# Kernel optimization log

Hardware: AMD Instinct MI355X
Metric: run time of the kernel (lower is better)

The kernel has to match this reference:

```python
import jax, jax.numpy as jnp
import numpy as np
import math

B, I, O, SEG = 128, 2048, 2048, 10

def setup_inputs() -> dict:
    key = jax.random.key(0)
    k1, k2, k3, k4 = jax.random.split(key, 4)
    scale = 1.0 / math.sqrt(I)
    return {
        "x": jax.random.normal(k1, (B, I), dtype=jnp.float32),
        "context": jax.random.normal(k2, (O,), dtype=jnp.float32),
        "prev_activation": jax.random.normal(k3, (B, O), dtype=jnp.float32),
        "weight": jax.random.normal(k4, (O, I), dtype=jnp.float32) * scale,
        "bias": jnp.zeros((O,), dtype=jnp.float32),
        "astrocyte_activation": jnp.ones((O,), dtype=jnp.float32),
        "dendrite_segments": jax.random.normal(jax.random.fold_in(key, 7), (O, I, SEG), dtype=jnp.float32) * scale,
    }

def reference(x, context, prev_activation, weight, bias, astrocyte_activation, dendrite_segments):
    # Astrocyte gating of the linear weight: sigmoid(astro * context) -> [o]
    astro_mod = jax.nn.sigmoid(astrocyte_activation * context)
    # Dendritic branch: relu(einsum('bi,oij->boj')) summed over segments -> [b, o]
    dendritic_out = jnp.maximum(jnp.einsum('bi,oij->boj', x, dendrite_segments), 0.0).sum(axis=2)
    # Gated linear: F.linear(x, weight * astro_mod[:, None], bias) -> [b, o]
    out = x @ (weight * astro_mod[:, None]).T + bias
    # Note: torch's STDP/Hebbian weight mutations (synaptic_tag, protein_synthesis,
    # homeostatic scaling) occur AFTER 'out' is computed and do not affect the
    # returned tensor; they are pure parameter side effects, so omitted here.
    return out + dendritic_out
```

## Files before the change

kernel.cpp:

```cpp
#include <hip/hip_runtime.h>
#include <hip/hip_bf16.h>

#define B_ 128
#define I_ 2048
#define O_ 2048
#define SEG 10
#define BK 32
#define NST (I_ / BK)
#define XTILE 8192
#define DCH 1280
#define DLS 1408

typedef __attribute__((ext_vector_type(8))) short bf16x8;
typedef __attribute__((ext_vector_type(4))) float f32x4;

static __device__ __forceinline__ unsigned short f2bf(float f) {
    unsigned u = __float_as_uint(f);
    u += 0x7FFFu + ((u >> 16) & 1u);
    return (unsigned short)(u >> 16);
}

static __device__ __forceinline__ unsigned cvt2(float lo, float hi) {
    __hip_bfloat162 h = __float22bfloat162_rn(make_float2(lo, hi));
    return *reinterpret_cast<unsigned*>(&h);
}

#define GLDS16(SRC, DST) \
    __builtin_amdgcn_global_load_lds( \
        (const __attribute__((address_space(1))) unsigned*)(SRC), \
        (__attribute__((address_space(3))) unsigned*)(DST), 16, 0, 0)
#define GLDS4(SRC, DST) \
    __builtin_amdgcn_global_load_lds( \
        (const __attribute__((address_space(1))) unsigned*)(SRC), \
        (__attribute__((address_space(3))) unsigned*)(DST), 4, 0, 0)

#define WAITVM(N) asm volatile("s_waitcnt vmcnt(" #N ")" ::: "memory")
#define BARRIER() do { __builtin_amdgcn_sched_barrier(0); \
                       __builtin_amdgcn_s_barrier(); \
                       __builtin_amdgcn_sched_barrier(0); } while (0)

__global__ void xconv(const float* __restrict__ x, char* __restrict__ xb) {
    int idx = blockIdx.x * 256 + threadIdx.x;
    int row = idx >> 8;
    int c   = idx & 255;
    int k0  = c * 8;
    int tt  = k0 >> 5;
    int kl  = k0 & 31;

    const float* xp = x + (size_t)row * I_ + k0;
    float4 a = *reinterpret_cast<const float4*>(xp);
    float4 b = *reinterpret_cast<const float4*>(xp + 4);

    bf16x8 h;
    h[0] = (short)f2bf(a.x); h[1] = (short)f2bf(a.y);
    h[2] = (short)f2bf(a.z); h[3] = (short)f2bf(a.w);
    h[4] = (short)f2bf(b.x); h[5] = (short)f2bf(b.y);
    h[6] = (short)f2bf(b.z); h[7] = (short)f2bf(b.w);

    int sw = ((row >> 1) & 3) << 4;
    size_t off = (size_t)tt * XTILE + row * 64 + ((kl * 2) ^ sw);
    *reinterpret_cast<bf16x8*>(xb + off) = h;
}

__global__ __launch_bounds__(256, 2) void neuro_fused(
    const char*  __restrict__ xb,
    const float* __restrict__ ctx,
    const float* __restrict__ w,
    const float* __restrict__ bias,
    const float* __restrict__ astro,
    const float* __restrict__ D,
    float* __restrict__ out)
{
    __shared__ __align__(16) char xs[4][XTILE];
    __shared__ __align__(16) char dls[4][4][DLS];

    const int tid  = threadIdx.x;
    const int wv   = tid >> 6;
    const int lane = tid & 63;
    const bool isP = (wv < 2);
    const int o0   = blockIdx.x * 4;
    const int col  = lane & 15;
    const int g    = lane >> 4;

    const int p = wv;
    auto stage_x = [&](int t) {
        const char* src = xb + (size_t)t * XTILE + p * 4096 + lane * 16;
        char* dst = &xs[t & 3][p * 4096];
#pragma unroll
        for (int c = 0; c < 4; ++c)
            GLDS16(src + c * 1024, dst + c * 1024);
    };
    auto stage_d = [&](int t) {
#pragma unroll
        for (int q = 0; q < 2; ++q) {
            const int ol = 2 * p + q;
            const char* srcD = (const char*)D + (size_t)(o0 + ol) * (I_ * SEG * 4)
                             + (size_t)t * DCH;
            char* dst = &dls[ol][t & 3][0];
            GLDS16(srcD + lane * 16, dst);
            GLDS4(srcD + 1024 + lane * 4, dst + 1024);
            const char* srcW = (const char*)w + (size_t)(o0 + ol) * (I_ * 4) + t * (BK * 4);
            if (lane < 32) GLDS4(srcW + lane * 4, dst + DCH);
        }
    };

    const int c_ = wv - 2;
    f32x4 acc[2][8];
#pragma unroll
    for (int oo = 0; oo < 2; ++oo)
#pragma unroll
        for (int m = 0; m < 8; ++m) acc[oo][m] = (f32x4){0.f, 0.f, 0.f, 0.f};

    float am[2], bo[2];
    if (!isP) {
#pragma unroll
        for (int oo = 0; oo < 2; ++oo) {
            const int o = o0 + 2 * c_ + oo;
            float a = astro[o] * ctx[o];
            am[oo] = 1.0f / (1.0f + __expf(-a));
            bo[oo] = bias[o];
        }
    }

    const int fbase = (col < 10) ? col * 4 : DCH;
    const int fstr  = (col < 10) ? 40 : 4;
    const int sw    = ((col >> 1) & 3) << 4;

    auto compute = [&](int u) {
        const char* xbase = &xs[u & 3][0];
        bf16x8 af[8];
#pragma unroll
        for (int m = 0; m < 8; ++m)
            af[m] = *reinterpret_cast<const bf16x8*>(
                xbase + (m * 16 + col) * 64 + ((16 * g) ^ sw));
#pragma unroll
        for (int oo = 0; oo < 2; ++oo) {
            const char* fp = &dls[2 * c_ + oo][u & 3][0] + fbase + (8 * g) * fstr;
            float bv[8];
#pragma unroll
            for (int e = 0; e < 8; ++e)
                bv[e] = *reinterpret_cast<const float*>(fp + e * fstr);
            union { bf16x8 v; unsigned uu[4]; } bf;
#pragma unroll
            for (int e2 = 0; e2 < 4; ++e2)
                bf.uu[e2] = cvt2(bv[2 * e2], bv[2 * e2 + 1]);
#pragma unroll
            for (int m = 0; m < 8; ++m)
                acc[oo][m] = __builtin_amdgcn_mfma_f32_16x16x32_bf16(af[m], bf.v, acc[oo][m], 0, 0, 0);
        }
    };

    if (isP) {
        stage_x(0); stage_d(0);
        stage_x(1); stage_d(1);
        stage_x(2); stage_d(2);
        WAITVM(20);
    }

#pragma unroll 1
    for (int u = 0; u < NST; ++u) {
        BARRIER();
        if (isP) {
            if (u + 3 < NST) { stage_x(u + 3); stage_d(u + 3); }
            if (u <= NST - 4)      { WAITVM(20); }
            else if (u == NST - 3) { WAITVM(10); }
            else                   { WAITVM(0);  }
        } else {
            compute(u);
        }
    }

    if (!isP) {
#pragma unroll
        for (int oo = 0; oo < 2; ++oo) {
            const int o = o0 + 2 * c_ + oo;
#pragma unroll
            for (int m = 0; m < 8; ++m) {
#pragma unroll
                for (int r = 0; r < 4; ++r) {
                    float v = acc[oo][m][r];
                    float dend = (col < 10) ? fmaxf(v, 0.0f) : 0.0f;
#pragma unroll
                    for (int sh = 1; sh < 16; sh <<= 1)
                        dend += __shfl_xor(dend, sh, 64);
                    float lin = __shfl(v, (lane & 48) | 10, 64);
                    if (col == 0) {
                        int b = m * 16 + g * 4 + r;
                        out[(size_t)b * O_ + o] = dend + am[oo] * lin + bo[oo];
                    }
                }
            }
        }
    }
}

extern "C" void kernel_launch(void* const* d_in, const int* in_sizes, int n_in,
                              void* d_out, int out_size, void* d_ws, size_t ws_size,
                              hipStream_t stream) {
    const float* x     = (const float*)d_in[0];
    const float* ctx   = (const float*)d_in[1];
    const float* w     = (const float*)d_in[3];
    const float* bias  = (const float*)d_in[4];
    const float* astro = (const float*)d_in[5];
    const float* D     = (const float*)d_in[6];
    float* out = (float*)d_out;
    char* xb = (char*)d_ws;

    xconv<<<dim3(128), dim3(256), 0, stream>>>(x, xb);
    neuro_fused<<<dim3(512), dim3(256), 0, stream>>>(xb, ctx, w, bias, astro, D, out);
}
```

Before: 48.94 us.

## Replace per-stage block barriers with LDS flag producer/consumer handshakes

The per-stage workgroup barrier is replaced by counters in LDS. The two loader waves publish how many stages are ready, and the two MFMA waves publish how many stages they have consumed. Each side spins with s_sleep on the other's counters, so producers and consumers are no longer locked to each other every iteration and can drift within the 4-deep ring. The cost is polling overhead on volatile LDS reads. Correctness also now relies on the vmcnt wait making the async LDS writes visible to the other waves before a flag is set, which a barrier used to guarantee.

```diff
diff --git a/kernel.cpp b/kernel.cpp
--- a/kernel.cpp
+++ b/kernel.cpp
@@ -35,9 +35,7 @@
         (__attribute__((address_space(3))) unsigned*)(DST), 4, 0, 0)
 
 #define WAITVM(N) asm volatile("s_waitcnt vmcnt(" #N ")" ::: "memory")
-#define BARRIER() do { __builtin_amdgcn_sched_barrier(0); \
-                       __builtin_amdgcn_s_barrier(); \
-                       __builtin_amdgcn_sched_barrier(0); } while (0)
+#define SB() __builtin_amdgcn_sched_barrier(0)
 
 __global__ void xconv(const float* __restrict__ x, char* __restrict__ xb) {
     int idx = blockIdx.x * 256 + threadIdx.x;
@@ -73,6 +71,7 @@
 {
     __shared__ __align__(16) char xs[4][XTILE];
     __shared__ __align__(16) char dls[4][4][DLS];
+    __shared__ int sflg[16];
 
     const int tid  = threadIdx.x;
     const int wv   = tid >> 6;
@@ -82,112 +81,133 @@
     const int col  = lane & 15;
     const int g    = lane >> 4;
 
-    const int p = wv;
-    auto stage_x = [&](int t) {
-        const char* src = xb + (size_t)t * XTILE + p * 4096 + lane * 16;
-        char* dst = &xs[t & 3][p * 4096];
-#pragma unroll
-        for (int c = 0; c < 4; ++c)
-            GLDS16(src + c * 1024, dst + c * 1024);
-    };
-    auto stage_d = [&](int t) {
-#pragma unroll
-        for (int q = 0; q < 2; ++q) {
-            const int ol = 2 * p + q;
-            const char* srcD = (const char*)D + (size_t)(o0 + ol) * (I_ * SEG * 4)
-                             + (size_t)t * DCH;
-            char* dst = &dls[ol][t & 3][0];
-            GLDS16(srcD + lane * 16, dst);
-            GLDS4(srcD + 1024 + lane * 4, dst + 1024);
-            const char* srcW = (const char*)w + (size_t)(o0 + ol) * (I_ * 4) + t * (BK * 4);
-            if (lane < 32) GLDS4(srcW + lane * 4, dst + DCH);
-        }
-    };
-
-    const int c_ = wv - 2;
-    f32x4 acc[2][8];
-#pragma unroll
-    for (int oo = 0; oo < 2; ++oo)
-#pragma unroll
-        for (int m = 0; m < 8; ++m) acc[oo][m] = (f32x4){0.f, 0.f, 0.f, 0.f};
-
-    float am[2], bo[2];
-    if (!isP) {
-#pragma unroll
-        for (int oo = 0; oo < 2; ++oo) {
-            const int o = o0 + 2 * c_ + oo;
-            float a = astro[o] * ctx[o];
-            am[oo] = 1.0f / (1.0f + __expf(-a));
-            bo[oo] = bias[o];
-        }
-    }
-
-    const int fbase = (col < 10) ? col * 4 : DCH;
-    const int fstr  = (col < 10) ? 40 : 4;
-    const int sw    = ((col >> 1) & 3) << 4;
-
-    auto compute = [&](int u) {
-        const char* xbase = &xs[u & 3][0];
-        bf16x8 af[8];
-#pragma unroll
-        for (int m = 0; m < 8; ++m)
-            af[m] = *reinterpret_cast<const bf16x8*>(
-                xbase + (m * 16 + col) * 64 + ((16 * g) ^ sw));
-#pragma unroll
-        for (int oo = 0; oo < 2; ++oo) {
-            const char* fp = &dls[2 * c_ + oo][u & 3][0] + fbase + (8 * g) * fstr;
-            float bv[8];
-#pragma unroll
-            for (int e = 0; e < 8; ++e)
-                bv[e] = *reinterpret_cast<const float*>(fp + e * fstr);
-            union { bf16x8 v; unsigned uu[4]; } bf;
-#pragma unroll
-            for (int e2 = 0; e2 < 4; ++e2)
-                bf.uu[e2] = cvt2(bv[2 * e2], bv[2 * e2 + 1]);
-#pragma unroll
-            for (int m = 0; m < 8; ++m)
-                acc[oo][m] = __builtin_amdgcn_mfma_f32_16x16x32_bf16(af[m], bf.v, acc[oo][m], 0, 0, 0);
-        }
-    };
+    if (tid < 16) sflg[tid] = 0;
+    __syncthreads();
 
     if (isP) {
+        const int p = wv;
+        auto stage_x = [&](int t) {
+            const char* src = xb + (size_t)t * XTILE + p * 4096 + lane * 16;
+            char* dst = &xs[t & 3][p * 4096];
+#pragma unroll
+            for (int c = 0; c < 4; ++c)
+                GLDS16(src + c * 1024, dst + c * 1024);
+        };
+        auto stage_d = [&](int t) {
+#pragma unroll
+            for (int q = 0; q < 2; ++q) {
+                const int ol = 2 * p + q;
+                const char* srcD = (const char*)D + (size_t)(o0 + ol) * (I_ * SEG * 4)
+                                 + (size_t)t * DCH;
+                char* dst = &dls[ol][t & 3][0];
+                GLDS16(srcD + lane * 16, dst);
+                GLDS4(srcD + 1024 + lane * 4, dst + 1024);
+                const char* srcW = (const char*)w + (size_t)(o0 + ol) * (I_ * 4) + t * (BK * 4);
+                if (lane < 32) GLDS4(srcW + lane * 4, dst + DCH);
+            }
+        };
+
         stage_x(0); stage_d(0);
         stage_x(1); stage_d(1);
         stage_x(2); stage_d(2);
-        WAITVM(20);
-    }
+
+        volatile int* vc0 = &sflg[8];
+        volatile int* vc1 = &sflg[12];
+        volatile int* myf = &sflg[p * 4];
 
 #pragma unroll 1
-    for (int u = 0; u < NST; ++u) {
-        BARRIER();
-        if (isP) {
+        for (int u = 0; u < NST; ++u) {
+            while (*vc0 < u || *vc1 < u) {
+                asm volatile("" ::: "memory");
+                __builtin_amdgcn_s_sleep(1);
+            }
+            SB();
             if (u + 3 < NST) { stage_x(u + 3); stage_d(u + 3); }
             if (u <= NST - 4)      { WAITVM(20); }
             else if (u == NST - 3) { WAITVM(10); }
             else                   { WAITVM(0);  }
-        } else {
-            compute(u);
-        }
-    }
-
-    if (!isP) {
+            SB();
+            if (lane == 0) *myf = u + 2;
+        }
+        return;
+    }
+
+    const int c_ = wv - 2;
+    f32x4 acc[2][8];
+#pragma unroll
+    for (int oo = 0; oo < 2; ++oo)
+#pragma unroll
+        for (int m = 0; m < 8; ++m) acc[oo][m] = (f32x4){0.f, 0.f, 0.f, 0.f};
+
+    float am[2], bo[2];
+#pragma unroll
+    for (int oo = 0; oo < 2; ++oo) {
+        const int o = o0 + 2 * c_ + oo;
+        float a = astro[o] * ctx[o];
+        am[oo] = 1.0f / (1.0f + __expf(-a));
+        bo[oo] = bias[o];
+    }
+
+    const int fbase = (col < 10) ? col * 4 : DCH;
+    const int fstr  = (col < 10) ? 40 : 4;
+    const int sw    = ((col >> 1) & 3) << 4;
+
+    auto compute = [&](int u) {
+        const char* xbase = &xs[u & 3][0];
+        bf16x8 af[8];
+#pragma unroll
+        for (int m = 0; m < 8; ++m)
+            af[m] = *reinterpret_cast<const bf16x8*>(
+                xbase + (m * 16 + col) * 64 + ((16 * g) ^ sw));
 #pragma unroll
         for (int oo = 0; oo < 2; ++oo) {
-            const int o = o0 + 2 * c_ + oo;
-#pragma unroll
-            for (int m = 0; m < 8; ++m) {
-#pragma unroll
-                for (int r = 0; r < 4; ++r) {
-                    float v = acc[oo][m][r];
-                    float dend = (col < 10) ? fmaxf(v, 0.0f) : 0.0f;
-#pragma unroll
-                    for (int sh = 1; sh < 16; sh <<= 1)
-                        dend += __shfl_xor(dend, sh, 64);
-                    float lin = __shfl(v, (lane & 48) | 10, 64);
-                    if (col == 0) {
-                        int b = m * 16 + g * 4 + r;
-                        out[(size_t)b * O_ + o] = dend + am[oo] * lin + bo[oo];
-                    }
+            const char* fp = &dls[2 * c_ + oo][u & 3][0] + fbase + (8 * g) * fstr;
+            float bv[8];
+#pragma unroll
+            for (int e = 0; e < 8; ++e)
+                bv[e] = *reinterpret_cast<const float*>(fp + e * fstr);
+            union { bf16x8 v; unsigned uu[4]; } bf;
+#pragma unroll
+            for (int e2 = 0; e2 < 4; ++e2)
+                bf.uu[e2] = cvt2(bv[2 * e2], bv[2 * e2 + 1]);
+#pragma unroll
+            for (int m = 0; m < 8; ++m)
+                acc[oo][m] = __builtin_amdgcn_mfma_f32_16x16x32_bf16(af[m], bf.v, acc[oo][m], 0, 0, 0);
+        }
+    };
+
+    volatile int* vf0 = &sflg[0];
+    volatile int* vf1 = &sflg[4];
+    volatile int* myc = &sflg[8 + c_ * 4];
+
+#pragma unroll 1
+    for (int u = 0; u < NST; ++u) {
+        while (*vf0 < u + 1 || *vf1 < u + 1) {
+            asm volatile("" ::: "memory");
+            __builtin_amdgcn_s_sleep(1);
+        }
+        SB();
+        compute(u);
+        SB();
+        if (lane == 0) *myc = u + 1;
+    }
+
+#pragma unroll
+    for (int oo = 0; oo < 2; ++oo) {
+        const int o = o0 + 2 * c_ + oo;
+#pragma unroll
+        for (int m = 0; m < 8; ++m) {
+#pragma unroll
+            for (int r = 0; r < 4; ++r) {
+                float v = acc[oo][m][r];
+                float dend = (col < 10) ? fmaxf(v, 0.0f) : 0.0f;
+#pragma unroll
+                for (int sh = 1; sh < 16; sh <<= 1)
+                    dend += __shfl_xor(dend, sh, 64);
+                float lin = __shfl(v, (lane & 48) | 10, 64);
+                if (col == 0) {
+                    int b = m * 16 + g * 4 + r;
+                    out[(size_t)b * O_ + o] = dend + am[oo] * lin + bo[oo];
                 }
             }
         }
```

Result: slower. 67.85 us (+38.6%).

## Double K-tile to 64 and widen blocks to 8 outputs with 8 waves

Applied to the files above, without the earlier changes.

Raises the K step per pipeline stage from 32 to 64 and makes each block handle 8 output neurons with 4 producer and 4 consumer waves (512 threads, 256 blocks). This halves the number of barrier-synchronised stages and shares each staged x tile across twice as many outputs. The x layout swizzle and the wait counts are adjusted to match. LDS use grows to about 155 KB and occupancy drops to one block per CU, so less latency is hidden by parallel blocks.

```diff
diff --git a/kernel.cpp b/kernel.cpp
--- a/kernel.cpp
+++ b/kernel.cpp
@@ -5,11 +5,12 @@
 #define I_ 2048
 #define O_ 2048
 #define SEG 10
-#define BK 32
+#define BK 64
 #define NST (I_ / BK)
-#define XTILE 8192
-#define DCH 1280
-#define DLS 1408
+#define XT 16384
+#define DCH 2560
+#define DSL 2816
+#define DEPTH 4
 
 typedef __attribute__((ext_vector_type(8))) short bf16x8;
 typedef __attribute__((ext_vector_type(4))) float f32x4;
@@ -44,8 +45,8 @@
     int row = idx >> 8;
     int c   = idx & 255;
     int k0  = c * 8;
-    int tt  = k0 >> 5;
-    int kl  = k0 & 31;
+    int tt  = k0 >> 6;
+    int kl  = k0 & 63;
 
     const float* xp = x + (size_t)row * I_ + k0;
     float4 a = *reinterpret_cast<const float4*>(xp);
@@ -57,12 +58,11 @@
     h[4] = (short)f2bf(b.x); h[5] = (short)f2bf(b.y);
     h[6] = (short)f2bf(b.z); h[7] = (short)f2bf(b.w);
 
-    int sw = ((row >> 1) & 3) << 4;
-    size_t off = (size_t)tt * XTILE + row * 64 + ((kl * 2) ^ sw);
+    size_t off = (size_t)tt * XT + row * 128 + ((kl * 2) ^ ((row & 7) << 4));
     *reinterpret_cast<bf16x8*>(xb + off) = h;
 }
 
-__global__ __launch_bounds__(256, 2) void neuro_fused(
+__global__ __launch_bounds__(512, 1) void neuro_fused(
     const char*  __restrict__ xb,
     const float* __restrict__ ctx,
     const float* __restrict__ w,
@@ -71,20 +71,20 @@
     const float* __restrict__ D,
     float* __restrict__ out)
 {
-    __shared__ __align__(16) char xs[4][XTILE];
-    __shared__ __align__(16) char dls[4][4][DLS];
+    __shared__ __align__(16) char xs[DEPTH][XT];
+    __shared__ __align__(16) char dls[8][DEPTH][DSL];
 
     const int tid  = threadIdx.x;
     const int wv   = tid >> 6;
     const int lane = tid & 63;
-    const bool isP = (wv < 2);
-    const int o0   = blockIdx.x * 4;
+    const bool isP = (wv < 4);
+    const int o0   = blockIdx.x * 8;
     const int col  = lane & 15;
     const int g    = lane >> 4;
 
     const int p = wv;
     auto stage_x = [&](int t) {
-        const char* src = xb + (size_t)t * XTILE + p * 4096 + lane * 16;
+        const char* src = xb + (size_t)t * XT + p * 4096 + lane * 16;
         char* dst = &xs[t & 3][p * 4096];
 #pragma unroll
         for (int c = 0; c < 4; ++c)
@@ -98,13 +98,15 @@
                              + (size_t)t * DCH;
             char* dst = &dls[ol][t & 3][0];
             GLDS16(srcD + lane * 16, dst);
-            GLDS4(srcD + 1024 + lane * 4, dst + 1024);
+            GLDS16(srcD + 1024 + lane * 16, dst + 1024);
+            GLDS4(srcD + 2048 + lane * 4, dst + 2048);
+            GLDS4(srcD + 2304 + lane * 4, dst + 2304);
             const char* srcW = (const char*)w + (size_t)(o0 + ol) * (I_ * 4) + t * (BK * 4);
-            if (lane < 32) GLDS4(srcW + lane * 4, dst + DCH);
+            GLDS4(srcW + lane * 4, dst + DCH);
         }
     };
 
-    const int c_ = wv - 2;
+    const int c_ = wv - 4;
     f32x4 acc[2][8];
 #pragma unroll
     for (int oo = 0; oo < 2; ++oo)
@@ -124,29 +126,38 @@
 
     const int fbase = (col < 10) ? col * 4 : DCH;
     const int fstr  = (col < 10) ? 40 : 4;
-    const int sw    = ((col >> 1) & 3) << 4;
-
-    auto compute = [&](int u) {
-        const char* xbase = &xs[u & 3][0];
-        bf16x8 af[8];
-#pragma unroll
-        for (int m = 0; m < 8; ++m)
-            af[m] = *reinterpret_cast<const bf16x8*>(
-                xbase + (m * 16 + col) * 64 + ((16 * g) ^ sw));
+    const int sw    = (col & 7) << 4;
+
+    auto compute = [&](int t) {
+        const char* xbase = &xs[t & 3][0];
+        bf16x8 af[2][8];
+#pragma unroll
+        for (int kk = 0; kk < 2; ++kk) {
+            const int kswz = (kk * 64 + 16 * g) ^ sw;
+#pragma unroll
+            for (int m = 0; m < 8; ++m)
+                af[kk][m] = *reinterpret_cast<const bf16x8*>(
+                    xbase + (m * 16 + col) * 128 + kswz);
+        }
 #pragma unroll
         for (int oo = 0; oo < 2; ++oo) {
-            const char* fp = &dls[2 * c_ + oo][u & 3][0] + fbase + (8 * g) * fstr;
-            float bv[8];
-#pragma unroll
-            for (int e = 0; e < 8; ++e)
-                bv[e] = *reinterpret_cast<const float*>(fp + e * fstr);
-            union { bf16x8 v; unsigned uu[4]; } bf;
-#pragma unroll
-            for (int e2 = 0; e2 < 4; ++e2)
-                bf.uu[e2] = cvt2(bv[2 * e2], bv[2 * e2 + 1]);
-#pragma unroll
-            for (int m = 0; m < 8; ++m)
-                acc[oo][m] = __builtin_amdgcn_mfma_f32_16x16x32_bf16(af[m], bf.v, acc[oo][m], 0, 0, 0);
+            const char* dbase = &dls[2 * c_ + oo][t & 3][0] + fbase;
+#pragma unroll
+            for (int kk = 0; kk < 2; ++kk) {
+                const char* fp = dbase + (32 * kk + 8 * g) * fstr;
+                float bv[8];
+#pragma unroll
+                for (int e = 0; e < 8; ++e)
+                    bv[e] = *reinterpret_cast<const float*>(fp + e * fstr);
+                union { bf16x8 v; unsigned uu[4]; } bf;
+#pragma unroll
+                for (int e2 = 0; e2 < 4; ++e2)
+                    bf.uu[e2] = cvt2(bv[2 * e2], bv[2 * e2 + 1]);
+#pragma unroll
+                for (int m = 0; m < 8; ++m)
+                    acc[oo][m] = __builtin_amdgcn_mfma_f32_16x16x32_bf16(
+                        af[kk][m], bf.v, acc[oo][m], 0, 0, 0);
+            }
         }
     };
 
@@ -154,19 +165,19 @@
         stage_x(0); stage_d(0);
         stage_x(1); stage_d(1);
         stage_x(2); stage_d(2);
-        WAITVM(20);
+        WAITVM(28);
     }
 
 #pragma unroll 1
-    for (int u = 0; u < NST; ++u) {
+    for (int t = 0; t < NST; ++t) {
         BARRIER();
         if (isP) {
-            if (u + 3 < NST) { stage_x(u + 3); stage_d(u + 3); }
-            if (u <= NST - 4)      { WAITVM(20); }
-            else if (u == NST - 3) { WAITVM(10); }
-            else                   { WAITVM(0);  }
+            if (t + 3 < NST) { stage_x(t + 3); stage_d(t + 3); }
+            if (t <= NST - 4)      { WAITVM(28); }
+            else if (t == NST - 3) { WAITVM(14); }
+            else if (t == NST - 2) { WAITVM(0);  }
         } else {
-            compute(u);
+            compute(t);
         }
     }
 
@@ -207,5 +218,5 @@
     char* xb = (char*)d_ws;
 
     xconv<<<dim3(128), dim3(256), 0, stream>>>(x, xb);
-    neuro_fused<<<dim3(512), dim3(256), 0, stream>>>(xb, ctx, w, bias, astro, D, out);
-}
+    neuro_fused<<<dim3(256), dim3(512), 0, stream>>>(xb, ctx, w, bias, astro, D, out);
+}
```

New measurement: 49.62 us. Within noise of the previous version (+1.4%).

## Load x fragments directly to registers and stage D in larger super-steps

Applied to the files above, without the earlier changes.

The x tile no longer passes through LDS. Consumer waves load bf16 x fragments straight from global (L2) into registers, double-buffered so the next tile's load overlaps the current tile's MFMAs. Producer waves now stage four K-tiles of dendrite and weight data per super-step, using 16-byte loads into a 3-slot ring, which cuts the number of barriers by a factor of four and frees LDS. The risk is extra global/L2 traffic for x on every block and possible latency exposure on the register loads, and the xb swizzle is dropped.

```diff
diff --git a/kernel.cpp b/kernel.cpp
--- a/kernel.cpp
+++ b/kernel.cpp
@@ -5,11 +5,11 @@
 #define I_ 2048
 #define O_ 2048
 #define SEG 10
-#define BK 32
-#define NST (I_ / BK)
+#define NSS 16
+#define NT 64
 #define XTILE 8192
-#define DCH 1280
-#define DLS 1408
+#define SSB 5120
+#define SLOT 5632
 
 typedef __attribute__((ext_vector_type(8))) short bf16x8;
 typedef __attribute__((ext_vector_type(4))) float f32x4;
@@ -29,10 +29,6 @@
     __builtin_amdgcn_global_load_lds( \
         (const __attribute__((address_space(1))) unsigned*)(SRC), \
         (__attribute__((address_space(3))) unsigned*)(DST), 16, 0, 0)
-#define GLDS4(SRC, DST) \
-    __builtin_amdgcn_global_load_lds( \
-        (const __attribute__((address_space(1))) unsigned*)(SRC), \
-        (__attribute__((address_space(3))) unsigned*)(DST), 4, 0, 0)
 
 #define WAITVM(N) asm volatile("s_waitcnt vmcnt(" #N ")" ::: "memory")
 #define BARRIER() do { __builtin_amdgcn_sched_barrier(0); \
@@ -57,8 +53,7 @@
     h[4] = (short)f2bf(b.x); h[5] = (short)f2bf(b.y);
     h[6] = (short)f2bf(b.z); h[7] = (short)f2bf(b.w);
 
-    int sw = ((row >> 1) & 3) << 4;
-    size_t off = (size_t)tt * XTILE + row * 64 + ((kl * 2) ^ sw);
+    size_t off = (size_t)tt * XTILE + row * 64 + kl * 2;
     *reinterpret_cast<bf16x8*>(xb + off) = h;
 }
 
@@ -71,8 +66,7 @@
     const float* __restrict__ D,
     float* __restrict__ out)
 {
-    __shared__ __align__(16) char xs[4][XTILE];
-    __shared__ __align__(16) char dls[4][4][DLS];
+    __shared__ __align__(16) char dls[4][3][SLOT];
 
     const int tid  = threadIdx.x;
     const int wv   = tid >> 6;
@@ -82,27 +76,35 @@
     const int col  = lane & 15;
     const int g    = lane >> 4;
 
-    const int p = wv;
-    auto stage_x = [&](int t) {
-        const char* src = xb + (size_t)t * XTILE + p * 4096 + lane * 16;
-        char* dst = &xs[t & 3][p * 4096];
-#pragma unroll
-        for (int c = 0; c < 4; ++c)
-            GLDS16(src + c * 1024, dst + c * 1024);
-    };
-    auto stage_d = [&](int t) {
-#pragma unroll
-        for (int q = 0; q < 2; ++q) {
-            const int ol = 2 * p + q;
-            const char* srcD = (const char*)D + (size_t)(o0 + ol) * (I_ * SEG * 4)
-                             + (size_t)t * DCH;
-            char* dst = &dls[ol][t & 3][0];
-            GLDS16(srcD + lane * 16, dst);
-            GLDS4(srcD + 1024 + lane * 4, dst + 1024);
-            const char* srcW = (const char*)w + (size_t)(o0 + ol) * (I_ * 4) + t * (BK * 4);
-            if (lane < 32) GLDS4(srcW + lane * 4, dst + DCH);
+    if (isP) {
+        const int p = wv;
+        auto stage = [&](int S) {
+#pragma unroll
+            for (int q = 0; q < 2; ++q) {
+                const int ol = 2 * p + q;
+                const char* srcD = (const char*)D + (size_t)(o0 + ol) * (I_ * SEG * 4)
+                                 + (size_t)S * SSB;
+                char* dst = &dls[ol][S % 3][0];
+#pragma unroll
+                for (int c = 0; c < 5; ++c)
+                    GLDS16(srcD + c * 1024 + lane * 16, dst + c * 1024);
+                const char* srcW = (const char*)w + (size_t)(o0 + ol) * (I_ * 4) + S * 512;
+                if (lane < 32) GLDS16(srcW + lane * 16, dst + SSB);
+            }
+        };
+
+        stage(0); stage(1);
+        WAITVM(12);
+
+#pragma unroll 1
+        for (int S = 0; S < NSS; ++S) {
+            BARRIER();
+            if (S + 2 < NSS) stage(S + 2);
+            if (S <= NSS - 3) { WAITVM(12); }
+            else              { WAITVM(0);  }
         }
-    };
+        return;
+    }
 
     const int c_ = wv - 2;
     f32x4 acc[2][8];
@@ -112,30 +114,33 @@
         for (int m = 0; m < 8; ++m) acc[oo][m] = (f32x4){0.f, 0.f, 0.f, 0.f};
 
     float am[2], bo[2];
-    if (!isP) {
+#pragma unroll
+    for (int oo = 0; oo < 2; ++oo) {
+        const int o = o0 + 2 * c_ + oo;
+        float a = astro[o] * ctx[o];
+        am[oo] = 1.0f / (1.0f + __expf(-a));
+        bo[oo] = bias[o];
+    }
+
+    const int boff = (col < 10) ? (col * 4 + g * 320) : (SSB + g * 32);
+    const int bmul = (col < 10) ? 1280 : 128;
+    const int fstr = (col < 10) ? 40 : 4;
+
+    const char* asrc = xb + col * 64 + g * 16;
+
+    auto issueA = [&](int t, bf16x8 (&dst)[8]) {
+        const char* src = asrc + (size_t)t * XTILE;
+#pragma unroll
+        for (int m = 0; m < 8; ++m)
+            dst[m] = *reinterpret_cast<const bf16x8*>(src + m * 1024);
+    };
+
+    auto compute = [&](int t, bf16x8 (&af)[8]) {
+        const int slot = (t >> 2) % 3;
+        const int fb   = boff + (t & 3) * bmul;
 #pragma unroll
         for (int oo = 0; oo < 2; ++oo) {
-            const int o = o0 + 2 * c_ + oo;
-            float a = astro[o] * ctx[o];
-            am[oo] = 1.0f / (1.0f + __expf(-a));
-            bo[oo] = bias[o];
-        }
-    }
-
-    const int fbase = (col < 10) ? col * 4 : DCH;
-    const int fstr  = (col < 10) ? 40 : 4;
-    const int sw    = ((col >> 1) & 3) << 4;
-
-    auto compute = [&](int u) {
-        const char* xbase = &xs[u & 3][0];
-        bf16x8 af[8];
-#pragma unroll
-        for (int m = 0; m < 8; ++m)
-            af[m] = *reinterpret_cast<const bf16x8*>(
-                xbase + (m * 16 + col) * 64 + ((16 * g) ^ sw));
-#pragma unroll
-        for (int oo = 0; oo < 2; ++oo) {
-            const char* fp = &dls[2 * c_ + oo][u & 3][0] + fbase + (8 * g) * fstr;
+            const char* fp = &dls[2 * c_ + oo][slot][0] + fb;
             float bv[8];
 #pragma unroll
             for (int e = 0; e < 8; ++e)
@@ -150,44 +155,36 @@
         }
     };
 
-    if (isP) {
-        stage_x(0); stage_d(0);
-        stage_x(1); stage_d(1);
-        stage_x(2); stage_d(2);
-        WAITVM(20);
-    }
+    bf16x8 afA[8], afB[8];
+    issueA(0, afA);
 
 #pragma unroll 1
-    for (int u = 0; u < NST; ++u) {
+    for (int S = 0; S < NSS; ++S) {
         BARRIER();
-        if (isP) {
-            if (u + 3 < NST) { stage_x(u + 3); stage_d(u + 3); }
-            if (u <= NST - 4)      { WAITVM(20); }
-            else if (u == NST - 3) { WAITVM(10); }
-            else                   { WAITVM(0);  }
-        } else {
-            compute(u);
-        }
-    }
-
-    if (!isP) {
-#pragma unroll
-        for (int oo = 0; oo < 2; ++oo) {
-            const int o = o0 + 2 * c_ + oo;
-#pragma unroll
-            for (int m = 0; m < 8; ++m) {
-#pragma unroll
-                for (int r = 0; r < 4; ++r) {
-                    float v = acc[oo][m][r];
-                    float dend = (col < 10) ? fmaxf(v, 0.0f) : 0.0f;
-#pragma unroll
-                    for (int sh = 1; sh < 16; sh <<= 1)
-                        dend += __shfl_xor(dend, sh, 64);
-                    float lin = __shfl(v, (lane & 48) | 10, 64);
-                    if (col == 0) {
-                        int b = m * 16 + g * 4 + r;
-                        out[(size_t)b * O_ + o] = dend + am[oo] * lin + bo[oo];
-                    }
+        const int t0 = 4 * S;
+        issueA(t0 + 1, afB);  compute(t0,     afA);
+        issueA(t0 + 2, afA);  compute(t0 + 1, afB);
+        issueA(t0 + 3, afB);  compute(t0 + 2, afA);
+        if (t0 + 4 < NT) issueA(t0 + 4, afA);
+        compute(t0 + 3, afB);
+    }
+
+#pragma unroll
+    for (int oo = 0; oo < 2; ++oo) {
+        const int o = o0 + 2 * c_ + oo;
+#pragma unroll
+        for (int m = 0; m < 8; ++m) {
+#pragma unroll
+            for (int r = 0; r < 4; ++r) {
+                float v = acc[oo][m][r];
+                float dend = (col < 10) ? fmaxf(v, 0.0f) : 0.0f;
+#pragma unroll
+                for (int sh = 1; sh < 16; sh <<= 1)
+                    dend += __shfl_xor(dend, sh, 64);
+                float lin = __shfl(v, (lane & 48) | 10, 64);
+                if (col == 0) {
+                    int b = m * 16 + g * 4 + r;
+                    out[(size_t)b * O_ + o] = dend + am[oo] * lin + bo[oo];
                 }
             }
         }
```

After: 70.74 us. +44.5%, slower.
